# Performance work log

Measured on AMD Instinct MI355X. Metric: run time of the kernel, lower is better.

Reference implementation:

```python
import jax, jax.numpy as jnp
import numpy as np

NUM_HEADS = 8
KERNEL_SEARCH = 5  # local attention window
EPS = 1e-5


def _layernorm(x, g, b):
    m = jnp.mean(x, axis=-1, keepdims=True)
    v = jnp.var(x, axis=-1, keepdims=True)
    return (x - m) / jnp.sqrt(v + EPS) * g + b


def _unfold3(x):
    # x: [N, C, H, W] -> [N, C*9, H*W]; matches torch F.unfold(kernel=3, pad=1)
    # ordering: channel-major, kernel position (row-major) minor.
    N, C, H, W = x.shape
    xp = jnp.pad(x, ((0, 0), (0, 0), (1, 1), (1, 1)))
    pats = jnp.stack([xp[:, :, i:i + H, j:j + W] for i in range(3) for j in range(3)], axis=2)
    return pats.reshape(N, C * 9, H * W)


def _sai2token(x, w_mlp):
    # x: [b, c, a, h, w] -> tokens [h*w, b*a, spa_dim]
    b, c, a, h, w = x.shape
    x = x.transpose(0, 2, 1, 3, 4).reshape(b * a, c, h, w)
    tok = _unfold3(x).transpose(2, 0, 1)  # [hw, b*a, c*9]
    return jnp.einsum('lnk,ek->lne', tok, w_mlp)


def _local_mask(h, w, k):
    # additive mask [h*w, h*w]: 0 inside local kxk window, -inf outside
    kl, kr = k // 2, k - k // 2
    ii = jnp.arange(h)
    jj = jnp.arange(w)
    okh = (ii[None, :] >= ii[:, None] - kl) & (ii[None, :] < ii[:, None] + kr)  # [h,h]
    okw = (jj[None, :] >= jj[:, None] - kl) & (jj[None, :] < jj[:, None] + kr)  # [w,w]
    ok = okh[:, None, :, None] & okw[None, :, None, :]  # [h,w,h,w]
    ok = ok.reshape(h * w, h * w)
    return jnp.where(ok, 0.0, -jnp.inf).astype(jnp.float32)


def _attention(qk_in, v_in, in_proj_w, out_proj_w, bias):
    # qk_in/v_in: [L, B, E]; torch nn.MultiheadAttention, no biases, eval mode
    L, B, E = qk_in.shape
    Dh = E // NUM_HEADS
    Wq, Wk, Wv = in_proj_w[:E], in_proj_w[E:2 * E], in_proj_w[2 * E:]
    q = jnp.einsum('lbe,fe->lbf', qk_in, Wq).reshape(L, B, NUM_HEADS, Dh)
    k = jnp.einsum('lbe,fe->lbf', qk_in, Wk).reshape(L, B, NUM_HEADS, Dh)
    v = jnp.einsum('lbe,fe->lbf', v_in, Wv).reshape(L, B, NUM_HEADS, Dh)
    scale = 1.0 / np.sqrt(Dh).astype(np.float32)
    scores = jnp.einsum('lbhd,mbhd->bhlm', q, k) * scale + bias[None, None]
    attn = jax.nn.softmax(scores, axis=-1)
    out = jnp.einsum('bhlm,mbhd->lbhd', attn, v).reshape(L, B, E)
    return jnp.einsum('lbe,fe->lbf', out, out_proj_w)


def reference(buffer, spa_position, w_mlp, ln1_g, ln1_b, in_proj_w, out_proj_w,
              ln2_g, ln2_b, ff_w1, ff_w2, conv_w):
    b, c, a, h, w = buffer.shape
    bias = _local_mask(h, w, KERNEL_SEARCH)
    tok = _sai2token(buffer, w_mlp)          # [hw, b*a, E]
    pe = _sai2token(spa_position, w_mlp)
    x = _layernorm(tok + pe, ln1_g, ln1_b)
    tok = _attention(x, tok, in_proj_w, out_proj_w, bias) + tok
    # feed-forward (dropout is identity in eval)
    ff = _layernorm(tok, ln2_g, ln2_b)
    ff = jax.nn.relu(jnp.einsum('lbe,fe->lbf', ff, ff_w1))
    tok = jnp.einsum('lbf,ef->lbe', ff, ff_w2) + tok
    # Token2SAI: '(h w) (b a) e -> b e a h w' then 1x1x1 conv3d
    buf = tok.reshape(h, w, b, a, -1).transpose(2, 4, 3, 0, 1)  # [b, E, a, h, w]
    return jnp.einsum('oe,beahw->boahw', conv_w, buf)


def setup_inputs() -> dict:
    key = jax.random.key(0)
    ks = jax.random.split(key, 8)
    b, c, a, h, w = 1, 64, 25, 32, 32
    E = 2 * c
    s = 0.02
    return {
        'buffer': jax.random.normal(ks[0], (b, c, a, h, w), jnp.float32),
        'spa_position': jax.random.normal(ks[1], (b, c, a, h, w), jnp.float32),
        'w_mlp': jax.random.normal(ks[2], (E, c * 9), jnp.float32) * s,
        'ln1_g': jnp.ones((E,), jnp.float32),
        'ln1_b': jnp.zeros((E,), jnp.float32),
        'in_proj_w': jax.random.normal(ks[3], (3 * E, E), jnp.float32) * s,
        'out_proj_w': jax.random.normal(ks[4], (E, E), jnp.float32) * s,
        'ln2_g': jnp.ones((E,), jnp.float32),
        'ln2_b': jnp.zeros((E,), jnp.float32),
        'ff_w1': jax.random.normal(ks[5], (2 * E, E), jnp.float32) * s,
        'ff_w2': jax.random.normal(ks[6], (E, 2 * E), jnp.float32) * s,
        'conv_w': jax.random.normal(ks[7], (c, E), jnp.float32) * s,
    }
```

## Files before the change

### kernel.cpp

```cpp
#include <hip/hip_runtime.h>
#include <math.h>

#define Lh 32
#define Lw 32
#define LL 1024
#define BN 25
#define EE 128
#define CC 64
#define NHD 8
#define DH 16
#define FFD 256
#define MROWS 25600

typedef __attribute__((ext_vector_type(8))) short short8;
typedef __attribute__((ext_vector_type(4))) float f32x4;

__device__ inline ushort f2b(float x) {
    union { float f; unsigned u; } v; v.f = x;
    unsigned r = (v.u + 0x7fffu + ((v.u >> 16) & 1u)) >> 16;
    return (ushort)r;
}
__device__ inline float b2f(ushort u) {
    union { unsigned u; float f; } v; v.u = ((unsigned)u) << 16;
    return v.f;
}

#define OFF_W2  0
#define OFF_WQK 73728
#define OFF_WV  106496
#define OFF_WO  122880
#define OFF_W1  139264
#define OFF_W2F 172032
#define OFF_WC  204800
#define W_TOTAL 212992

__global__ __launch_bounds__(256) void k_prep(
    const float* __restrict__ w_mlp, const float* __restrict__ in_proj,
    const float* __restrict__ out_proj, const float* __restrict__ ff_w1,
    const float* __restrict__ ff_w2, const float* __restrict__ conv_w,
    ushort* __restrict__ Wb)
{
    int i = blockIdx.x * 256 + threadIdx.x;
    if (i >= W_TOTAL) return;
    if (i < 73728) {
        int e = i / 576, k = i - e * 576;
        int tap = k >> 6, ch = k & 63;
        Wb[OFF_W2 + i] = f2b(w_mlp[e * 576 + ch * 9 + tap]);
        return;
    }
    i -= 73728;
    if (i < 32768) {
        float v = in_proj[i];
        Wb[OFF_WQK + i] = f2b(i < 16384 ? v * 0.25f : v);
        return;
    }
    i -= 32768;
    if (i < 16384) { Wb[OFF_WV + i] = f2b(in_proj[32768 + i]); return; }
    i -= 16384;
    if (i < 16384) {
        int e = i >> 7, kpos = i & 127;
        int c = kpos >> 5, q = (kpos >> 3) & 3, ii = kpos & 7;
        int orig = (2 * c + (ii >> 2)) * 16 + q * 4 + (ii & 3);
        Wb[OFF_WO + i] = f2b(out_proj[e * 128 + orig]);
        return;
    }
    i -= 16384;
    if (i < 32768) { Wb[OFF_W1 + i] = f2b(ff_w1[i]); return; }
    i -= 32768;
    if (i < 32768) {
        int e = i >> 8, kpos = i & 255;
        int c = kpos >> 5, q = (kpos >> 3) & 3, ii = kpos & 7;
        int orig = (2 * c + (ii >> 2)) * 16 + q * 4 + (ii & 3);
        Wb[OFF_W2F + i] = f2b(ff_w2[e * 256 + orig]);
        return;
    }
    i -= 32768;
    {
        int o = i >> 7, kpos = i & 127;
        int c = kpos >> 5, q = (kpos >> 3) & 3, ii = kpos & 7;
        int orig = (2 * c + (ii >> 2)) * 16 + q * 4 + (ii & 3);
        Wb[OFF_WC + i] = f2b(conv_w[o * 128 + orig]);
    }
}

__global__ __launch_bounds__(256) void k_tok_qkv(
    const float* __restrict__ buf, const float* __restrict__ spa,
    const ushort* __restrict__ W2, const ushort* __restrict__ WQK,
    const ushort* __restrict__ WV, const float* __restrict__ g1,
    const float* __restrict__ b1, ushort* __restrict__ TOKb,
    ushort* __restrict__ Qh, ushort* __restrict__ Kh, ushort* __restrict__ VTg)
{
    const int bid = blockIdx.x;
    const int idx = (bid & 7) * 100 + (bid >> 3);
    const int n = idx / 32, y = idx & 31;
    __shared__ ushort At[3 * 34 * 72];
    __shared__ ushort As_[3 * 34 * 72];
    __shared__ ushort Xs[32 * 136];
    __shared__ ushort Vs[32 * 136];
    __shared__ float2 red[32][4];
    float* t0 = (float*)Xs;
    float* t1 = (float*)Vs;
    const int t = threadIdx.x;
    const uint4 z = make_uint4(0, 0, 0, 0);

    for (int dy = 0; dy < 3; dy++) {
        int yy = y + dy - 1;
        if (yy >= 0 && yy < Lh) {
            {
                int ch = t >> 2, x8 = (t & 3) * 8;
                const float* p = buf + ((size_t)(ch * BN + n) * LL + yy * Lw + x8);
                const float* q = spa + ((size_t)(ch * BN + n) * LL + yy * Lw + x8);
                float4 a0 = ((const float4*)p)[0], a1 = ((const float4*)p)[1];
                float4 b0 = ((const float4*)q)[0], b1 = ((const float4*)q)[1];
                float* d0 = t0 + ch * 33 + x8;
                float* d1 = t1 + ch * 33 + x8;
                d0[0] = a0.x; d0[1] = a0.y; d0[2] = a0.z; d0[3] = a0.w;
                d0[4] = a1.x; d0[5] = a1.y; d0[6] = a1.z; d0[7] = a1.w;
                d1[0] = a0.x + b0.x; d1[1] = a0.y + b0.y; d1[2] = a0.z + b0.z; d1[3] = a0.w + b0.w;
                d1[4] = a1.x + b1.x; d1[5] = a1.y + b1.y; d1[6] = a1.z + b1.z; d1[7] = a1.w + b1.w;
            }
            __syncthreads();
            {
                int x = t >> 3, c8 = (t & 7) * 8;
                union { ushort u[8]; uint4 v; } o0, o1;
#pragma unroll
                for (int j = 0; j < 8; j++) {
                    o0.u[j] = f2b(t0[(c8 + j) * 33 + x]);
                    o1.u[j] = f2b(t1[(c8 + j) * 33 + x]);
                }
                *(uint4*)(At + (dy * 34 + x + 1) * 72 + c8) = o0.v;
                *(uint4*)(As_ + (dy * 34 + x + 1) * 72 + c8) = o1.v;
            }
            __syncthreads();
        } else {
            int x = t >> 3, c8 = (t & 7) * 8;
            *(uint4*)(At + (dy * 34 + x + 1) * 72 + c8) = z;
            *(uint4*)(As_ + (dy * 34 + x + 1) * 72 + c8) = z;
        }
    }
    if (t < 48) {
        int dy = t / 16, rem = t % 16;
        int colp = (rem >> 3) * 33, c8p = (rem & 7) * 8;
        *(uint4*)(At + (dy * 34 + colp) * 72 + c8p) = z;
        *(uint4*)(As_ + (dy * 34 + colp) * 72 + c8p) = z;
    }
    __syncthreads();

    const int w = t >> 6, lane = t & 63;
    const int col = lane & 15, quad = lane >> 4;
    f32x4 accT[2][2] = {}, accS[2][2] = {};

    for (int tap = 0; tap < 9; tap++) {
        int dy = tap / 3, dx = tap % 3;
#pragma unroll
        for (int cc = 0; cc < 2; cc++) {
            int kg = tap * 64 + cc * 32 + quad * 8;
            short8 b0 = *(const short8*)(W2 + (size_t)(w * 32 + col) * 576 + kg);
            short8 bq = *(const short8*)(W2 + (size_t)(w * 32 + 16 + col) * 576 + kg);
            int abase = (dy * 34 + col + dx) * 72 + cc * 32 + quad * 8;
            short8 aT0 = *(const short8*)(At + abase);
            short8 aT1 = *(const short8*)(At + abase + 16 * 72);
            short8 aS0 = *(const short8*)(As_ + abase);
            short8 aS1 = *(const short8*)(As_ + abase + 16 * 72);
            accT[0][0] = __builtin_amdgcn_mfma_f32_16x16x32_bf16(aT0, b0, accT[0][0], 0, 0, 0);
            accT[0][1] = __builtin_amdgcn_mfma_f32_16x16x32_bf16(aT0, bq, accT[0][1], 0, 0, 0);
            accT[1][0] = __builtin_amdgcn_mfma_f32_16x16x32_bf16(aT1, b0, accT[1][0], 0, 0, 0);
            accT[1][1] = __builtin_amdgcn_mfma_f32_16x16x32_bf16(aT1, bq, accT[1][1], 0, 0, 0);
            accS[0][0] = __builtin_amdgcn_mfma_f32_16x16x32_bf16(aS0, b0, accS[0][0], 0, 0, 0);
            accS[0][1] = __builtin_amdgcn_mfma_f32_16x16x32_bf16(aS0, bq, accS[0][1], 0, 0, 0);
            accS[1][0] = __builtin_amdgcn_mfma_f32_16x16x32_bf16(aS1, b0, accS[1][0], 0, 0, 0);
            accS[1][1] = __builtin_amdgcn_mfma_f32_16x16x32_bf16(aS1, bq, accS[1][1], 0, 0, 0);
        }
    }

#pragma unroll
    for (int mi = 0; mi < 2; mi++)
#pragma unroll
        for (int r = 0; r < 4; r++) {
            float a0 = accS[mi][0][r], a1 = accS[mi][1][r];
            float ss = a0 + a1, qq = a0 * a0 + a1 * a1;
#pragma unroll
            for (int m = 1; m < 16; m <<= 1) {
                ss += __shfl_xor(ss, m, 64);
                qq += __shfl_xor(qq, m, 64);
            }
            if (col == 0) red[mi * 16 + quad * 4 + r][w] = make_float2(ss, qq);
        }
    __syncthreads();

    const float ga = g1[w * 32 + col],      ba = b1[w * 32 + col];
    const float gb = g1[w * 32 + 16 + col], bb = b1[w * 32 + 16 + col];
#pragma unroll
    for (int mi = 0; mi < 2; mi++)
#pragma unroll
        for (int r = 0; r < 4; r++) {
            int x = mi * 16 + quad * 4 + r;
            float2 p0 = red[x][0], p1 = red[x][1], p2 = red[x][2], p3 = red[x][3];
            float mean = (p0.x + p1.x + p2.x + p3.x) * (1.f / 128.f);
            float var  = (p0.y + p1.y + p2.y + p3.y) * (1.f / 128.f) - mean * mean;
            float rstd = rsqrtf(var + 1e-5f);
            int e0 = w * 32 + col, e1 = w * 32 + 16 + col;
            Xs[x * 136 + e0] = f2b((accS[mi][0][r] - mean) * rstd * ga + ba);
            Xs[x * 136 + e1] = f2b((accS[mi][1][r] - mean) * rstd * gb + bb);
            Vs[x * 136 + e0] = f2b(accT[mi][0][r]);
            Vs[x * 136 + e1] = f2b(accT[mi][1][r]);
        }
    __syncthreads();

    short8 xb[2][4], xv[2][4];
#pragma unroll
    for (int j = 0; j < 2; j++)
#pragma unroll
        for (int kc = 0; kc < 4; kc++) {
            xb[j][kc] = *(const short8*)(Xs + (j * 16 + col) * 136 + kc * 32 + quad * 8);
            xv[j][kc] = *(const short8*)(Vs + (j * 16 + col) * 136 + kc * 32 + quad * 8);
        }
    f32x4 Q[2][2] = {}, K[2][2] = {}, V[2][2] = {};
#pragma unroll
    for (int hj = 0; hj < 2; hj++) {
        int h = 2 * w + hj;
#pragma unroll
        for (int kc = 0; kc < 4; kc++) {
            short8 aq = *(const short8*)(WQK + (size_t)(h * 16 + col) * 128 + kc * 32 + quad * 8);
            short8 ak = *(const short8*)(WQK + (size_t)(128 + h * 16 + col) * 128 + kc * 32 + quad * 8);
            short8 av = *(const short8*)(WV + (size_t)(h * 16 + col) * 128 + kc * 32 + quad * 8);
#pragma unroll
            for (int j = 0; j < 2; j++) {
                Q[hj][j] = __builtin_amdgcn_mfma_f32_16x16x32_bf16(aq, xb[j][kc], Q[hj][j], 0, 0, 0);
                K[hj][j] = __builtin_amdgcn_mfma_f32_16x16x32_bf16(ak, xb[j][kc], K[hj][j], 0, 0, 0);
                V[hj][j] = __builtin_amdgcn_mfma_f32_16x16x32_bf16(av, xv[j][kc], V[hj][j], 0, 0, 0);
            }
        }
    }
    ushort* VTs = At;
#pragma unroll
    for (int hj = 0; hj < 2; hj++) {
        int h = 2 * w + hj;
#pragma unroll
        for (int j = 0; j < 2; j++) {
            int l = y * 32 + j * 16 + col;
            size_t base = ((size_t)(n * 8 + h) * 1024 + l) * 16 + quad * 4;
            ushort4 oq, ok;
            oq.x = f2b(Q[hj][j][0]); oq.y = f2b(Q[hj][j][1]); oq.z = f2b(Q[hj][j][2]); oq.w = f2b(Q[hj][j][3]);
            ok.x = f2b(K[hj][j][0]); ok.y = f2b(K[hj][j][1]); ok.z = f2b(K[hj][j][2]); ok.w = f2b(K[hj][j][3]);
            *(ushort4*)(Qh + base) = oq;
            *(ushort4*)(Kh + base) = ok;
            int xp = ((col >> 2) << 3) + (j << 2) + (col & 3);
#pragma unroll
            for (int r = 0; r < 4; r++)
                VTs[(h * 16 + quad * 4 + r) * 34 + xp] = f2b(V[hj][j][r]);
        }
    }
#pragma unroll
    for (int k = 0; k < 2; k++) {
        int idx2 = t + k * 256;
        int r = idx2 >> 4, seg = idx2 & 15;
        *(uint4*)(TOKb + ((size_t)((y * 32 + r) * 25 + n)) * 128 + seg * 8) =
            *(const uint4*)(Vs + r * 136 + seg * 8);
    }
    __syncthreads();
    {
        int h = t >> 5, rem = t & 31, d = rem >> 1, xh = (rem & 1) * 16;
        size_t vrow = ((size_t)(n * 8 + h) * 32 + y) * 512;
        union { ushort u[8]; uint4 v; } o0, o1;
#pragma unroll
        for (int j = 0; j < 8; j++) {
            o0.u[j] = VTs[(h * 16 + d) * 34 + xh + j];
            o1.u[j] = VTs[(h * 16 + d) * 34 + xh + 8 + j];
        }
        *(uint4*)(VTg + vrow + d * 32 + xh)     = o0.v;
        *(uint4*)(VTg + vrow + d * 32 + xh + 8) = o1.v;
    }
}

__global__ __launch_bounds__(256) void k_attn_ffn(
    const ushort* __restrict__ Qh, const ushort* __restrict__ Kh,
    const ushort* __restrict__ VTg, const ushort* __restrict__ WOP,
    const float* __restrict__ g2, const float* __restrict__ b2,
    const ushort* __restrict__ W1, const ushort* __restrict__ W2P,
    const ushort* __restrict__ WCP, const ushort* __restrict__ TOKb,
    float* __restrict__ out)
{
    __shared__ ushort OX[16 * 136];
    __shared__ ushort Rs[16 * 136];
    __shared__ ushort Hs[16 * 264];
    __shared__ ushort Ys[16 * 136];
    __shared__ float2 red[16][4];
    const int bid = blockIdx.x;
    const int idx = (bid & 7) * 200 + (bid >> 3);
    const int n = idx / 64, rem = idx & 63;
    const int y = rem >> 1, half = rem & 1;
    const int l0 = y * 32 + half * 16;
    const int t = threadIdx.x, w = t >> 6, lane = t & 63;
    const int col = lane & 15, quad = lane >> 4;
    const int qx = half * 16 + col;

    {
        int r = t >> 4, seg = t & 15;
        *(uint4*)(Rs + r * 136 + seg * 8) =
            *(const uint4*)(TOKb + ((size_t)((l0 + r) * 25 + n)) * 128 + seg * 8);
    }

    unsigned long long mbits = 0;
#pragma unroll
    for (int tt = 0; tt < 10; tt++) {
        int yy = y - 2 + (tt >> 1);
        bool rok = (yy >= 0) && (yy < 32);
        int kxb = ((tt & 1) << 4) + quad * 4;
#pragma unroll
        for (int r = 0; r < 4; r++) {
            int dd = kxb + r - qx;
            if (rok && ((unsigned)(dd + 2) <= 4u))
                mbits |= 1ull << (tt * 4 + r);
        }
    }

    short8 z8 = {0, 0, 0, 0, 0, 0, 0, 0};
    f32x4 O2[2] = {};
#pragma unroll
    for (int hj = 0; hj < 2; hj++) {
        const int h = 2 * w + hj;
        const size_t base = (size_t)(n * 8 + h) * 1024;
        const size_t vbase = ((size_t)(n * 8 + h) * 32) * 512;

        short8 qf = z8;
        if (quad < 2)
            qf = *(const short8*)(Qh + (base + y * 32 + half * 16 + col) * 16 + quad * 8);

        f32x4 Sc[10] = {};
#pragma unroll
        for (int tt = 0; tt < 10; tt++) {
            int kr = tt >> 1, kx = ((tt & 1) << 4) + col;
            int yyc = min(max(y - 2 + kr, 0), 31);
            short8 kf = z8;
            if (quad < 2)
                kf = *(const short8*)(Kh + (base + yyc * 32 + kx) * 16 + quad * 8);
            Sc[tt] = __builtin_amdgcn_mfma_f32_16x16x32_bf16(kf, qf, Sc[tt], 0, 0, 0);
        }

        float mx = -1e30f;
#pragma unroll
        for (int tt = 0; tt < 10; tt++)
#pragma unroll
            for (int r = 0; r < 4; r++) {
                bool ok = (mbits >> (tt * 4 + r)) & 1;
                float v = ok ? Sc[tt][r] : -1e30f;
                Sc[tt][r] = v;
                mx = fmaxf(mx, v);
            }
        mx = fmaxf(mx, __shfl_xor(mx, 16, 64));
        mx = fmaxf(mx, __shfl_xor(mx, 32, 64));
        float sum = 0.f;
#pragma unroll
        for (int tt = 0; tt < 10; tt++)
#pragma unroll
            for (int r = 0; r < 4; r++) {
                float p = __expf(Sc[tt][r] - mx);
                Sc[tt][r] = p;
                sum += p;
            }
        sum += __shfl_xor(sum, 16, 64);
        sum += __shfl_xor(sum, 32, 64);
        const float inv = 1.f / sum;

#pragma unroll
        for (int c = 0; c < 5; c++) {
            int yyc = min(max(y - 2 + c, 0), 31);
            short8 vt = *(const short8*)(VTg + vbase + (size_t)yyc * 512 + col * 32 + quad * 8);
            union { ushort u[8]; short8 s; } pb;
#pragma unroll
            for (int i = 0; i < 8; i++)
                pb.u[i] = f2b(Sc[2 * c + (i >> 2)][i & 3]);
            O2[hj] = __builtin_amdgcn_mfma_f32_16x16x32_bf16(vt, pb.s, O2[hj], 0, 0, 0);
        }
#pragma unroll
        for (int r = 0; r < 4; r++) O2[hj][r] *= inv;
    }

    {
        union { ushort u[8]; uint4 v; } pb;
#pragma unroll
        for (int i = 0; i < 8; i++)
            pb.u[i] = f2b(O2[i >> 2][i & 3]);
        *(uint4*)(OX + col * 136 + w * 32 + quad * 8) = pb.v;
    }
    __syncthreads();

    f32x4 Y[2] = {};
#pragma unroll
    for (int kc = 0; kc < 4; kc++) {
        short8 hb = *(const short8*)(OX + col * 136 + kc * 32 + quad * 8);
#pragma unroll
        for (int jj = 0; jj < 2; jj++) {
            int et = 2 * w + jj;
            short8 a = *(const short8*)(WOP + (size_t)(et * 16 + col) * 128 + kc * 32 + quad * 8);
            Y[jj] = __builtin_amdgcn_mfma_f32_16x16x32_bf16(a, hb, Y[jj], 0, 0, 0);
        }
    }
    float sum = 0.f, sq = 0.f;
#pragma unroll
    for (int jj = 0; jj < 2; jj++)
#pragma unroll
        for (int r = 0; r < 4; r++) {
            int e = (2 * w + jj) * 16 + quad * 4 + r;
            float v = Y[jj][r] + b2f(Rs[col * 136 + e]);
            Y[jj][r] = v;
            sum += v; sq += v * v;
        }
    sum += __shfl_xor(sum, 16, 64); sum += __shfl_xor(sum, 32, 64);
    sq  += __shfl_xor(sq, 16, 64);  sq  += __shfl_xor(sq, 32, 64);
    if (quad == 0) red[col][w] = make_float2(sum, sq);
    __syncthreads();

    {
        float2 p0 = red[col][0], p1 = red[col][1], p2 = red[col][2], p3 = red[col][3];
        float mean = (p0.x + p1.x + p2.x + p3.x) * (1.f / 128.f);
        float var  = (p0.y + p1.y + p2.y + p3.y) * (1.f / 128.f) - mean * mean;
        float rstd = rsqrtf(var + 1e-5f);
#pragma unroll
        for (int jj = 0; jj < 2; jj++)
#pragma unroll
            for (int r = 0; r < 4; r++) {
                int e = (2 * w + jj) * 16 + quad * 4 + r;
                OX[col * 136 + e] = f2b((Y[jj][r] - mean) * rstd * g2[e] + b2[e]);
            }
    }
    __syncthreads();

    short8 xb[4];
#pragma unroll
    for (int kc = 0; kc < 4; kc++)
        xb[kc] = *(const short8*)(OX + col * 136 + kc * 32 + quad * 8);
    f32x4 H[4] = {};
#pragma unroll
    for (int j = 0; j < 4; j++) {
        int ft = 4 * w + j;
#pragma unroll
        for (int kc = 0; kc < 4; kc++) {
            short8 a = *(const short8*)(W1 + (size_t)(ft * 16 + col) * 128 + kc * 32 + quad * 8);
            H[j] = __builtin_amdgcn_mfma_f32_16x16x32_bf16(a, xb[kc], H[j], 0, 0, 0);
        }
    }
#pragma unroll
    for (int cc = 0; cc < 2; cc++) {
        union { ushort u[8]; uint4 v; } pb;
#pragma unroll
        for (int i = 0; i < 8; i++)
            pb.u[i] = f2b(fmaxf(H[2 * cc + (i >> 2)][i & 3], 0.f));
        *(uint4*)(Hs + col * 264 + (2 * w + cc) * 32 + quad * 8) = pb.v;
    }
    __syncthreads();

    f32x4 Y2[2] = {};
#pragma unroll
    for (int kc = 0; kc < 8; kc++) {
        short8 hb = *(const short8*)(Hs + col * 264 + kc * 32 + quad * 8);
#pragma unroll
        for (int j = 0; j < 2; j++) {
            int et = 2 * w + j;
            short8 a = *(const short8*)(W2P + (size_t)(et * 16 + col) * 256 + kc * 32 + quad * 8);
            Y2[j] = __builtin_amdgcn_mfma_f32_16x16x32_bf16(a, hb, Y2[j], 0, 0, 0);
        }
    }
    {
        union { ushort u[8]; uint4 v; } pb;
#pragma unroll
        for (int i = 0; i < 8; i++)
            pb.u[i] = f2b(Y2[i >> 2][i & 3] + Y[i >> 2][i & 3]);
        *(uint4*)(Ys + col * 136 + w * 32 + quad * 8) = pb.v;
    }
    __syncthreads();

    f32x4 O = {};
#pragma unroll
    for (int c = 0; c < 4; c++) {
        short8 yb = *(const short8*)(Ys + col * 136 + c * 32 + quad * 8);
        short8 a = *(const short8*)(WCP + (size_t)(w * 16 + col) * 128 + c * 32 + quad * 8);
        O = __builtin_amdgcn_mfma_f32_16x16x32_bf16(a, yb, O, 0, 0, 0);
    }
    const int l = l0 + col;
#pragma unroll
    for (int r2 = 0; r2 < 4; r2++) {
        int o = w * 16 + quad * 4 + r2;
        out[(size_t)(o * 25 + n) * 1024 + l] = O[r2];
    }
}

extern "C" void kernel_launch(void* const* d_in, const int* in_sizes, int n_in,
                              void* d_out, int out_size, void* d_ws, size_t ws_size,
                              hipStream_t stream)
{
    const float* buffer   = (const float*)d_in[0];
    const float* spa      = (const float*)d_in[1];
    const float* w_mlp    = (const float*)d_in[2];
    const float* ln1_g    = (const float*)d_in[3];
    const float* ln1_b    = (const float*)d_in[4];
    const float* in_proj  = (const float*)d_in[5];
    const float* out_proj = (const float*)d_in[6];
    const float* ln2_g    = (const float*)d_in[7];
    const float* ln2_b    = (const float*)d_in[8];
    const float* ff_w1    = (const float*)d_in[9];
    const float* ff_w2    = (const float*)d_in[10];
    const float* conv_w   = (const float*)d_in[11];
    float* out = (float*)d_out;

    char* ws = (char*)d_ws;
    ushort* TOKb = (ushort*)(ws);
    ushort* Qh   = (ushort*)(ws + 6553600);
    ushort* Kh   = (ushort*)(ws + 13107200);
    ushort* VTg  = (ushort*)(ws + 19660800);
    ushort* Wb   = (ushort*)(ws + 26214400);

    k_prep<<<dim3((W_TOTAL + 255) / 256), 256, 0, stream>>>(
        w_mlp, in_proj, out_proj, ff_w1, ff_w2, conv_w, Wb);
    k_tok_qkv<<<dim3(800), 256, 0, stream>>>(buffer, spa, Wb + OFF_W2,
                                             Wb + OFF_WQK, Wb + OFF_WV,
                                             ln1_g, ln1_b, TOKb, Qh, Kh, VTg);
    k_attn_ffn<<<dim3(1600), 256, 0, stream>>>(Qh, Kh, VTg, Wb + OFF_WO,
                                               ln2_g, ln2_b, Wb + OFF_W1,
                                               Wb + OFF_W2F, Wb + OFF_WC,
                                               TOKb, out);
}
```

Measured before the change: 174.5 us.

## Interleave two attention heads, drop softmax max, alias LDS and raise occupancy hints

Both heads handled by a wave in the attention kernel are now processed together, so their K/V loads and MFMAs interleave for more instruction-level parallelism. The softmax no longer subtracts the row maximum, which removes the max pass and two shuffles. The Ys shared buffer now reuses Rs to cut LDS use, and launch-bounds min-blocks hints are added to both kernels. Dropping the max subtraction risks overflow in exp for large scores, and the larger live register set competes with the occupancy hints, which could cause spills.

New measurement: 172.4 us. No clear change (-1.2%).

```diff
diff --git a/kernel.cpp b/kernel.cpp
--- a/kernel.cpp
+++ b/kernel.cpp
@@ -83,7 +83,7 @@
     }
 }
 
-__global__ __launch_bounds__(256) void k_tok_qkv(
+__global__ __launch_bounds__(256, 3) void k_tok_qkv(
     const float* __restrict__ buf, const float* __restrict__ spa,
     const ushort* __restrict__ W2, const ushort* __restrict__ WQK,
     const ushort* __restrict__ WV, const float* __restrict__ g1,
@@ -273,7 +273,7 @@
     }
 }
 
-__global__ __launch_bounds__(256) void k_attn_ffn(
+__global__ __launch_bounds__(256, 4) void k_attn_ffn(
     const ushort* __restrict__ Qh, const ushort* __restrict__ Kh,
     const ushort* __restrict__ VTg, const ushort* __restrict__ WOP,
     const float* __restrict__ g2, const float* __restrict__ b2,
@@ -284,8 +284,8 @@
     __shared__ ushort OX[16 * 136];
     __shared__ ushort Rs[16 * 136];
     __shared__ ushort Hs[16 * 264];
-    __shared__ ushort Ys[16 * 136];
     __shared__ float2 red[16][4];
+    ushort* Ys = Rs;
     const int bid = blockIdx.x;
     const int idx = (bid & 7) * 200 + (bid >> 3);
     const int n = idx / 64, rem = idx & 63;
@@ -316,72 +316,68 @@
     }
 
     short8 z8 = {0, 0, 0, 0, 0, 0, 0, 0};
-    f32x4 O2[2] = {};
-#pragma unroll
-    for (int hj = 0; hj < 2; hj++) {
-        const int h = 2 * w + hj;
-        const size_t base = (size_t)(n * 8 + h) * 1024;
-        const size_t vbase = ((size_t)(n * 8 + h) * 32) * 512;
-
-        short8 qf = z8;
-        if (quad < 2)
-            qf = *(const short8*)(Qh + (base + y * 32 + half * 16 + col) * 16 + quad * 8);
-
-        f32x4 Sc[10] = {};
-#pragma unroll
-        for (int tt = 0; tt < 10; tt++) {
-            int kr = tt >> 1, kx = ((tt & 1) << 4) + col;
-            int yyc = min(max(y - 2 + kr, 0), 31);
-            short8 kf = z8;
-            if (quad < 2)
-                kf = *(const short8*)(Kh + (base + yyc * 32 + kx) * 16 + quad * 8);
-            Sc[tt] = __builtin_amdgcn_mfma_f32_16x16x32_bf16(kf, qf, Sc[tt], 0, 0, 0);
-        }
-
-        float mx = -1e30f;
-#pragma unroll
-        for (int tt = 0; tt < 10; tt++)
-#pragma unroll
-            for (int r = 0; r < 4; r++) {
-                bool ok = (mbits >> (tt * 4 + r)) & 1;
-                float v = ok ? Sc[tt][r] : -1e30f;
-                Sc[tt][r] = v;
-                mx = fmaxf(mx, v);
-            }
-        mx = fmaxf(mx, __shfl_xor(mx, 16, 64));
-        mx = fmaxf(mx, __shfl_xor(mx, 32, 64));
-        float sum = 0.f;
-#pragma unroll
-        for (int tt = 0; tt < 10; tt++)
-#pragma unroll
-            for (int r = 0; r < 4; r++) {
-                float p = __expf(Sc[tt][r] - mx);
-                Sc[tt][r] = p;
-                sum += p;
-            }
-        sum += __shfl_xor(sum, 16, 64);
-        sum += __shfl_xor(sum, 32, 64);
-        const float inv = 1.f / sum;
-
-#pragma unroll
-        for (int c = 0; c < 5; c++) {
-            int yyc = min(max(y - 2 + c, 0), 31);
-            short8 vt = *(const short8*)(VTg + vbase + (size_t)yyc * 512 + col * 32 + quad * 8);
-            union { ushort u[8]; short8 s; } pb;
-#pragma unroll
-            for (int i = 0; i < 8; i++)
-                pb.u[i] = f2b(Sc[2 * c + (i >> 2)][i & 3]);
-            O2[hj] = __builtin_amdgcn_mfma_f32_16x16x32_bf16(vt, pb.s, O2[hj], 0, 0, 0);
-        }
-#pragma unroll
-        for (int r = 0; r < 4; r++) O2[hj][r] *= inv;
-    }
+    const size_t base0 = (size_t)(n * 8 + 2 * w) * 1024;
+    const size_t base1 = base0 + 1024;
+    const size_t vbase0 = (size_t)(n * 8 + 2 * w) * 32 * 512;
+    const size_t vbase1 = vbase0 + 32 * 512;
+
+    short8 qf0 = z8, qf1 = z8;
+    if (quad < 2) {
+        qf0 = *(const short8*)(Qh + (base0 + y * 32 + half * 16 + col) * 16 + quad * 8);
+        qf1 = *(const short8*)(Qh + (base1 + y * 32 + half * 16 + col) * 16 + quad * 8);
+    }
+
+    f32x4 Sc[2][10] = {};
+#pragma unroll
+    for (int tt = 0; tt < 10; tt++) {
+        int kr = tt >> 1, kx = ((tt & 1) << 4) + col;
+        int yyc = min(max(y - 2 + kr, 0), 31);
+        short8 kf0 = z8, kf1 = z8;
+        if (quad < 2) {
+            kf0 = *(const short8*)(Kh + (base0 + yyc * 32 + kx) * 16 + quad * 8);
+            kf1 = *(const short8*)(Kh + (base1 + yyc * 32 + kx) * 16 + quad * 8);
+        }
+        Sc[0][tt] = __builtin_amdgcn_mfma_f32_16x16x32_bf16(kf0, qf0, Sc[0][tt], 0, 0, 0);
+        Sc[1][tt] = __builtin_amdgcn_mfma_f32_16x16x32_bf16(kf1, qf1, Sc[1][tt], 0, 0, 0);
+    }
+
+    float sum0 = 0.f, sum1 = 0.f;
+#pragma unroll
+    for (int tt = 0; tt < 10; tt++)
+#pragma unroll
+        for (int r = 0; r < 4; r++) {
+            bool ok = (mbits >> (tt * 4 + r)) & 1;
+            float p0 = ok ? __expf(Sc[0][tt][r]) : 0.f;
+            float p1 = ok ? __expf(Sc[1][tt][r]) : 0.f;
+            Sc[0][tt][r] = p0; Sc[1][tt][r] = p1;
+            sum0 += p0; sum1 += p1;
+        }
+    sum0 += __shfl_xor(sum0, 16, 64); sum0 += __shfl_xor(sum0, 32, 64);
+    sum1 += __shfl_xor(sum1, 16, 64); sum1 += __shfl_xor(sum1, 32, 64);
+    const float inv0 = 1.f / sum0, inv1 = 1.f / sum1;
+
+    f32x4 O20 = {}, O21 = {};
+#pragma unroll
+    for (int c = 0; c < 5; c++) {
+        int yyc = min(max(y - 2 + c, 0), 31);
+        short8 vt0 = *(const short8*)(VTg + vbase0 + (size_t)yyc * 512 + col * 32 + quad * 8);
+        short8 vt1 = *(const short8*)(VTg + vbase1 + (size_t)yyc * 512 + col * 32 + quad * 8);
+        union { ushort u[8]; short8 s; } pb0, pb1;
+#pragma unroll
+        for (int i = 0; i < 8; i++) {
+            pb0.u[i] = f2b(Sc[0][2 * c + (i >> 2)][i & 3]);
+            pb1.u[i] = f2b(Sc[1][2 * c + (i >> 2)][i & 3]);
+        }
+        O20 = __builtin_amdgcn_mfma_f32_16x16x32_bf16(vt0, pb0.s, O20, 0, 0, 0);
+        O21 = __builtin_amdgcn_mfma_f32_16x16x32_bf16(vt1, pb1.s, O21, 0, 0, 0);
+    }
+#pragma unroll
+    for (int r = 0; r < 4; r++) { O20[r] *= inv0; O21[r] *= inv1; }
 
     {
         union { ushort u[8]; uint4 v; } pb;
 #pragma unroll
-        for (int i = 0; i < 8; i++)
-            pb.u[i] = f2b(O2[i >> 2][i & 3]);
+        for (int i = 0; i < 4; i++) { pb.u[i] = f2b(O20[i]); pb.u[4 + i] = f2b(O21[i]); }
         *(uint4*)(OX + col * 136 + w * 32 + quad * 8) = pb.v;
     }
     __syncthreads();
```
